# Optimization experiments

Hardware: AMD Instinct MI355X
Metric: run time of the kernel (lower is better)

## Reference

```python
import jax, jax.numpy as jnp
import numpy as np

NUM_HEADS = 16
NUM_KV_HEADS = 4
HEAD_DIM = 128
TOP_K = 4
RMS_EPS = 1e-6
ROPE_THETA = 10000.0


def setup_inputs() -> dict:
    key = jax.random.key(0)
    ks = jax.random.split(key, 10)
    T, h, E, I, SI = 1024, 2048, 16, 512, 1024
    s = 0.02  # weight init scale for numerical sanity
    return {
        "hidden_states": jax.random.normal(ks[0], (T, h), jnp.float32),
        "residual": jax.random.normal(ks[1], (T, h), jnp.float32),
        "rms1_w": jnp.ones((h,), jnp.float32),
        "rms2_w": jnp.ones((h,), jnp.float32),
        "w_qkv": jax.random.normal(ks[2], (h, NUM_HEADS * HEAD_DIM + 2 * NUM_KV_HEADS * HEAD_DIM), jnp.float32) * s,
        "w_dense": jax.random.normal(ks[3], (NUM_HEADS * HEAD_DIM, h), jnp.float32) * s,
        "gate_w": jax.random.normal(ks[4], (h, E), jnp.float32) * s,
        "w13": jax.random.normal(ks[5], (E, h, 2 * I), jnp.float32) * s,
        "w2": jax.random.normal(ks[6], (E, I, h), jnp.float32) * s,
        "sw13": jax.random.normal(ks[7], (h, 2 * SI), jnp.float32) * s,
        "sw2": jax.random.normal(ks[8], (SI, h), jnp.float32) * s,
        "position_ids": jnp.arange(T, dtype=jnp.int32),
    }


def _rmsnorm(x, w, eps=RMS_EPS):
    var = jnp.mean(jnp.square(x), axis=-1, keepdims=True)
    return x * jax.lax.rsqrt(var + eps) * w


def _rope_neox(pos, x):
    # x: [T, H, D]; rotate-half (neox) style over full head_dim
    d = x.shape[-1]
    inv_freq = 1.0 / (ROPE_THETA ** (jnp.arange(0, d, 2, dtype=jnp.float32) / d))  # [d/2]
    ang = pos.astype(jnp.float32)[:, None] * inv_freq  # [T, d/2]
    cos = jnp.cos(ang)[:, None, :]  # [T, 1, d/2]
    sin = jnp.sin(ang)[:, None, :]
    x1, x2 = x[..., : d // 2], x[..., d // 2 :]
    return jnp.concatenate([x1 * cos - x2 * sin, x2 * cos + x1 * sin], axis=-1)


def reference(hidden_states, residual, rms1_w, rms2_w, w_qkv, w_dense,
              gate_w, w13, w2, sw13, sw2, position_ids):
    T, h = hidden_states.shape
    q_size = NUM_HEADS * HEAD_DIM
    kv_size = NUM_KV_HEADS * HEAD_DIM

    # --- input RMSNorm with fused residual add ---
    resid = hidden_states + residual
    x = _rmsnorm(resid, rms1_w)

    # --- attention ---
    qkv = x @ w_qkv
    q = qkv[:, :q_size].reshape(T, NUM_HEADS, HEAD_DIM)
    k = qkv[:, q_size : q_size + kv_size].reshape(T, NUM_KV_HEADS, HEAD_DIM)
    v = qkv[:, q_size + kv_size :].reshape(T, NUM_KV_HEADS, HEAD_DIM)
    q = _rope_neox(position_ids, q)
    k = _rope_neox(position_ids, k)
    rep = NUM_HEADS // NUM_KV_HEADS
    kr = jnp.repeat(k, rep, axis=1)  # [T, H, D]
    vr = jnp.repeat(v, rep, axis=1)
    scale = HEAD_DIM ** -0.5
    scores = jnp.einsum('thd,shd->hts', q, kr) * scale  # [H, T, T]
    causal = jnp.tril(jnp.ones((T, T), dtype=bool))
    scores = jnp.where(causal[None], scores, -1e9)
    probs = jax.nn.softmax(scores, axis=-1)
    ctx = jnp.einsum('hts,shd->thd', probs, vr).reshape(T, q_size)
    attn_out = ctx @ w_dense

    # --- post-attention RMSNorm with fused residual add ---
    resid2 = attn_out + resid
    x2 = _rmsnorm(resid2, rms2_w)

    # --- shared experts (SiLU-and-mul MLP) ---
    gu = x2 @ sw13
    sg, su = jnp.split(gu, 2, axis=-1)
    shared = (jax.nn.silu(sg) * su) @ sw2

    # --- MoE routing: softmax -> top-k -> renormalize ---
    E = gate_w.shape[1]
    router_probs = jax.nn.softmax(x2 @ gate_w, axis=-1)  # [T, E]
    topk_w, topk_ids = jax.lax.top_k(router_probs, TOP_K)
    topk_w = topk_w / jnp.sum(topk_w, axis=-1, keepdims=True)
    comb = jnp.zeros((T, E), x2.dtype).at[jnp.arange(T)[:, None], topk_ids].add(topk_w)

    # --- experts (dense grouped-GEMM equivalent, combined by routing weights) ---
    h_all = jnp.einsum('td,edf->etf', x2, w13)  # [E, T, 2I]
    eg, eu = jnp.split(h_all, 2, axis=-1)
    act = jax.nn.silu(eg) * eu  # [E, T, I]
    moe = jnp.einsum('etf,efh,te->th', act, w2, comb)

    return (moe + shared, resid2)
```

## Files before the change

### kernel.cpp

```cpp
#include <hip/hip_runtime.h>
#include <math.h>

#define HD 2048
#define NQH 16
#define NKVH 4
#define HEADD 128
#define QKVN 3072
#define NEXP 16
#define EI 512
#define SSI 1024
#define TOPK 4
#define TT 1024

typedef __bf16 bf16x8 __attribute__((ext_vector_type(8)));
typedef float f32x4 __attribute__((ext_vector_type(4)));
typedef unsigned short u16x8 __attribute__((ext_vector_type(8)));

static __device__ __forceinline__ unsigned short f2bf(float f) {
    union { float f; unsigned int u; } v; v.f = f;
    unsigned int r = v.u + 0x7fff + ((v.u >> 16) & 1);
    return (unsigned short)(r >> 16);
}

static __device__ __forceinline__ void gl_lds16(const unsigned short* g,
                                                unsigned short* l) {
    __builtin_amdgcn_global_load_lds(
        (const __attribute__((address_space(1))) unsigned int*)g,
        (__attribute__((address_space(3))) unsigned int*)l, 16, 0, 0);
}

__global__ __launch_bounds__(256) void add_rmsnorm_kernel(
    const float* __restrict__ a, const float* __restrict__ b,
    const float* __restrict__ w, float* __restrict__ resid_out,
    unsigned short* __restrict__ x_bf)
{
    int t = blockIdx.x;
    int tid = threadIdx.x;
    const float4* a4 = (const float4*)(a + (size_t)t * HD);
    const float4* b4 = b ? (const float4*)(b + (size_t)t * HD) : nullptr;
    float4* r4 = resid_out ? (float4*)(resid_out + (size_t)t * HD) : nullptr;
    const float4* w4 = (const float4*)w;

    float4 v[2];
    float ss = 0.f;
#pragma unroll
    for (int l = 0; l < 2; ++l) {
        int idx = tid + l * 256;
        float4 va = a4[idx];
        if (b4) {
            float4 vb = b4[idx];
            va.x += vb.x; va.y += vb.y; va.z += vb.z; va.w += vb.w;
        }
        if (r4) r4[idx] = va;
        v[l] = va;
        ss += va.x * va.x + va.y * va.y + va.z * va.z + va.w * va.w;
    }
    for (int off = 32; off > 0; off >>= 1) ss += __shfl_down(ss, off);
    __shared__ float red[4];
    int lane = tid & 63, wv = tid >> 6;
    if (lane == 0) red[wv] = ss;
    __syncthreads();
    if (tid == 0) {
        float s = red[0] + red[1] + red[2] + red[3];
        red[0] = rsqrtf(s / (float)HD + 1e-6f);
    }
    __syncthreads();
    float inv = red[0];
#pragma unroll
    for (int l = 0; l < 2; ++l) {
        int idx = tid + l * 256;
        float4 va = v[l], vw = w4[idx];
        ushort4 ob;
        ob.x = f2bf(va.x * inv * vw.x);
        ob.y = f2bf(va.y * inv * vw.y);
        ob.z = f2bf(va.z * inv * vw.z);
        ob.w = f2bf(va.w * inv * vw.w);
        ((ushort4*)(x_bf + (size_t)t * HD))[idx] = ob;
    }
}

__global__ __launch_bounds__(256) void transpose_convert(
    const float* __restrict__ in, unsigned short* __restrict__ out,
    int K, int N, long long strideIn, long long strideOut)
{
    __shared__ float tile[64][33];
    const int n0 = blockIdx.x * 32;
    const int k0 = blockIdx.y * 64;
    const float* ip = in + (size_t)blockIdx.z * strideIn;
    unsigned short* op = out + (size_t)blockIdx.z * strideOut;
    int tid = threadIdx.x;
    int c = (tid & 7) * 4;
#pragma unroll
    for (int i = 0; i < 2; ++i) {
        int r = (tid >> 3) + i * 32;
        float4 v = *(const float4*)(ip + (size_t)(k0 + r) * N + n0 + c);
        tile[r][c] = v.x; tile[r][c + 1] = v.y;
        tile[r][c + 2] = v.z; tile[r][c + 3] = v.w;
    }
    __syncthreads();
    int rr = tid >> 3;
    int kc = (tid & 7) * 8;
    u16x8 o;
#pragma unroll
    for (int j = 0; j < 8; ++j) o[j] = f2bf(tile[kc + j][rr]);
    *(u16x8*)(op + (size_t)(n0 + rr) * K + k0 + kc) = o;
}

#define SBK 64

__global__ __launch_bounds__(256) void gemm_splitk(
    const unsigned short* __restrict__ A, const unsigned short* __restrict__ B,
    float* __restrict__ Cpart, int M, int N, int Kc, int ldA, int ldB)
{
    __shared__ unsigned short As[2][128 * SBK];
    __shared__ unsigned short Bs[2][128 * SBK];

    const int tid = threadIdx.x;
    const int wave = tid >> 6;
    const int lane = tid & 63;
    const int wr = wave >> 1, wc = wave & 1;
    const int l15 = lane & 15;
    const int row0 = blockIdx.y * 128;
    const int col0 = blockIdx.x * 128;
    const int z = blockIdx.z;

    const unsigned short* Ap = A + (size_t)row0 * ldA + (size_t)z * Kc;
    const unsigned short* Bp = B + (size_t)col0 * ldB + (size_t)z * Kc;

    const int r_st = tid >> 3;
    const int q_st = tid & 7;
    const int csrc = (q_st ^ (r_st & 7)) << 3;

    f32x4 acc[4][4] = {};

    const int nsteps = Kc / SBK;

#define STAGE_SK(buf, k0s)                                                    \
    {                                                                         \
        _Pragma("unroll")                                                     \
        for (int i = 0; i < 4; ++i) {                                         \
            int rr = r_st + i * 32;                                           \
            gl_lds16(Ap + (size_t)rr * ldA + (k0s) + csrc,                    \
                     &As[buf][rr * SBK + q_st * 8]);                          \
            gl_lds16(Bp + (size_t)rr * ldB + (k0s) + csrc,                    \
                     &Bs[buf][rr * SBK + q_st * 8]);                          \
        }                                                                     \
    }

    STAGE_SK(0, 0);

    for (int s = 0; s < nsteps; ++s) {
        const int cur = s & 1;
        if (s + 1 < nsteps) {
            STAGE_SK(cur ^ 1, (s + 1) * SBK);
            asm volatile("s_waitcnt vmcnt(8)" ::: "memory");
        } else {
            asm volatile("s_waitcnt vmcnt(0)" ::: "memory");
        }
        __builtin_amdgcn_s_barrier();

#pragma unroll
        for (int half = 0; half < 2; ++half) {
            const int q = half * 4 + (lane >> 4);
            bf16x8 af[4], bfv[4];
#pragma unroll
            for (int i = 0; i < 4; ++i) {
                int R = wr * 64 + i * 16 + l15;
                af[i] = *(const bf16x8*)&As[cur][R * SBK + ((q ^ (R & 7)) << 3)];
            }
#pragma unroll
            for (int j = 0; j < 4; ++j) {
                int R = wc * 64 + j * 16 + l15;
                bfv[j] = *(const bf16x8*)&Bs[cur][R * SBK + ((q ^ (R & 7)) << 3)];
            }
#pragma unroll
            for (int mi = 0; mi < 4; ++mi)
#pragma unroll
                for (int nj = 0; nj < 4; ++nj)
                    acc[mi][nj] = __builtin_amdgcn_mfma_f32_16x16x32_bf16(
                        af[mi], bfv[nj], acc[mi][nj], 0, 0, 0);
        }
        __builtin_amdgcn_s_barrier();
    }

    float* Cp = Cpart + (size_t)z * M * N;
#pragma unroll
    for (int mi = 0; mi < 4; ++mi)
#pragma unroll
        for (int nj = 0; nj < 4; ++nj)
#pragma unroll
            for (int r = 0; r < 4; ++r) {
                int row = row0 + wr * 64 + mi * 16 + (lane >> 4) * 4 + r;
                int col = col0 + wc * 64 + nj * 16 + l15;
                Cp[(size_t)row * N + col] = acc[mi][nj][r];
            }
}

__global__ __launch_bounds__(256) void reduce_partials(
    const float* __restrict__ part, int ns, int n4,
    const float* __restrict__ add, float* __restrict__ out, int acc)
{
    const float4* p4 = (const float4*)part;
    const float4* a4 = (const float4*)add;
    float4* o4 = (float4*)out;
    for (int idx = blockIdx.x * 256 + threadIdx.x; idx < n4;
         idx += gridDim.x * 256) {
        float4 s = p4[idx];
        for (int z = 1; z < ns; ++z) {
            float4 q = p4[(size_t)z * n4 + idx];
            s.x += q.x; s.y += q.y; s.z += q.z; s.w += q.w;
        }
        if (add) {
            float4 q = a4[idx];
            s.x += q.x; s.y += q.y; s.z += q.z; s.w += q.w;
        }
        if (acc) {
            float4 q = o4[idx];
            s.x += q.x; s.y += q.y; s.z += q.z; s.w += q.w;
        }
        o4[idx] = s;
    }
}

__global__ __launch_bounds__(256) void reduce_swiglu(
    const float* __restrict__ part, int ns, unsigned short* __restrict__ out)
{
    int idx4 = blockIdx.x * 256 + threadIdx.x;
    int t = idx4 >> 8;
    int i4 = (idx4 & 255) * 4;
    const float4* pg = (const float4*)(part + (size_t)t * (2 * SSI) + i4);
    const float4* pu = (const float4*)(part + (size_t)t * (2 * SSI) + SSI + i4);
    float4 g = pg[0], u = pu[0];
    for (int z = 1; z < ns; ++z) {
        float4 g2 = *(const float4*)((const float*)pg + (size_t)z * TT * 2 * SSI);
        float4 u2 = *(const float4*)((const float*)pu + (size_t)z * TT * 2 * SSI);
        g.x += g2.x; g.y += g2.y; g.z += g2.z; g.w += g2.w;
        u.x += u2.x; u.y += u2.y; u.z += u2.z; u.w += u2.w;
    }
    ushort4 o;
    o.x = f2bf((g.x / (1.f + __expf(-g.x))) * u.x);
    o.y = f2bf((g.y / (1.f + __expf(-g.y))) * u.y);
    o.z = f2bf((g.z / (1.f + __expf(-g.z))) * u.z);
    o.w = f2bf((g.w / (1.f + __expf(-g.w))) * u.w);
    *(ushort4*)(out + (size_t)t * SSI + i4) = o;
}

__global__ __launch_bounds__(256) void build_lists(
    const float* __restrict__ comb, int* __restrict__ lists,
    int* __restrict__ slots, int* __restrict__ cnts)
{
    int e = blockIdx.x;
    int tid = threadIdx.x;
    __shared__ int sc[256];
    int loc[4];
    int c = 0;
#pragma unroll
    for (int j = 0; j < 4; ++j) {
        int t = tid * 4 + j;
        if (comb[(size_t)t * NEXP + e] > 0.f) loc[c++] = t;
    }
    sc[tid] = c;
    __syncthreads();
    for (int off = 1; off < 256; off <<= 1) {
        int v = (tid >= off) ? sc[tid - off] : 0;
        __syncthreads();
        sc[tid] += v;
        __syncthreads();
    }
    int base = sc[tid] - c;
    for (int i = 0; i < c; ++i) {
        int t = loc[i];
        int s = 0;
        for (int e2 = 0; e2 < e; ++e2)
            s += (comb[(size_t)t * NEXP + e2] > 0.f) ? 1 : 0;
        lists[e * TT + base + i] = t;
        slots[e * TT + base + i] = s;
    }
    if (tid == 255) cnts[e] = sc[255];
}

__global__ void scan_cnts(const int* __restrict__ cnts, int* __restrict__ bases)
{
    if (threadIdx.x == 0 && blockIdx.x == 0) {
        int a = 0;
        for (int e = 0; e < NEXP; ++e) { bases[e] = a; a += cnts[e]; }
        bases[NEXP] = a;
    }
}

__global__ __launch_bounds__(256) void moe_up_gather(
    const unsigned short* __restrict__ x2B,
    const unsigned short* __restrict__ w13T,
    const float* __restrict__ comb,
    const int* __restrict__ lists,
    const int* __restrict__ cnts,
    const int* __restrict__ bases,
    unsigned short* __restrict__ actC)
{
    __shared__ unsigned short As[3][64 * 64];
    __shared__ unsigned short Bgs[3][64 * 64];
    __shared__ unsigned short Bus[3][64 * 64];

    const int e = blockIdx.z;
    const int cnt = cnts[e];
    const int m0 = blockIdx.y * 64;
    if (m0 >= cnt) return;
    const int n0 = blockIdx.x * 64;
    const int base_e = bases[e];

    const int tid = threadIdx.x;
    const int w = tid >> 6;
    const int lane = tid & 63;
    const int l15 = lane & 15;
    const int g = lane >> 4;

    const int r0 = tid >> 3;
    const int q_st = tid & 7;
    const int swz = (q_st ^ (r0 & 7)) << 3;

    int a0 = m0 + r0, a1 = m0 + r0 + 32;
    int tok0 = lists[e * TT + (a0 < cnt ? a0 : cnt - 1)];
    int tok1 = lists[e * TT + (a1 < cnt ? a1 : cnt - 1)];
    const unsigned short* Asrc0 = x2B + (size_t)tok0 * HD;
    const unsigned short* Asrc1 = x2B + (size_t)tok1 * HD;
    const unsigned short* Bbase = w13T + (size_t)e * 1024 * HD;
    const unsigned short* Bg0 = Bbase + (size_t)(n0 + r0) * HD;
    const unsigned short* Bg1 = Bbase + (size_t)(n0 + r0 + 32) * HD;
    const unsigned short* Bu0 = Bg0 + (size_t)512 * HD;
    const unsigned short* Bu1 = Bg1 + (size_t)512 * HD;

    f32x4 ag[4] = {};
    f32x4 au[4] = {};

#define STAGE_UP(buf, k0s)                                                    \
    {                                                                         \
        gl_lds16(Asrc0 + (k0s) + swz, &As[buf][(tid) * 8]);                   \
        gl_lds16(Asrc1 + (k0s) + swz, &As[buf][(tid + 256) * 8]);             \
        gl_lds16(Bg0 + (k0s) + swz, &Bgs[buf][(tid) * 8]);                    \
        gl_lds16(Bg1 + (k0s) + swz, &Bgs[buf][(tid + 256) * 8]);              \
        gl_lds16(Bu0 + (k0s) + swz, &Bus[buf][(tid) * 8]);                    \
        gl_lds16(Bu1 + (k0s) + swz, &Bus[buf][(tid + 256) * 8]);              \
    }

    const int nsteps = HD / 64;
    STAGE_UP(0, 0);
    STAGE_UP(1, 64);

    for (int s = 0; s < nsteps; ++s) {
        const int cur = s % 3;
        if (s + 2 < nsteps) {
            STAGE_UP((s + 2) % 3, (s + 2) * 64);
            asm volatile("s_waitcnt vmcnt(12)" ::: "memory");
        } else if (s + 1 < nsteps) {
            asm volatile("s_waitcnt vmcnt(6)" ::: "memory");
        } else {
            asm volatile("s_waitcnt vmcnt(0)" ::: "memory");
        }
        __builtin_amdgcn_s_barrier();

#pragma unroll
        for (int kk2 = 0; kk2 < 2; ++kk2) {
            const int q = kk2 * 4 + g;
            bf16x8 af[4], bg, bu;
#pragma unroll
            for (int i = 0; i < 4; ++i) {
                int R = i * 16 + l15;
                af[i] = *(const bf16x8*)&As[cur][R * 64 + ((q ^ (R & 7)) << 3)];
            }
            {
                int R = w * 16 + l15;
                int off = R * 64 + ((q ^ (R & 7)) << 3);
                bg = *(const bf16x8*)&Bgs[cur][off];
                bu = *(const bf16x8*)&Bus[cur][off];
            }
#pragma unroll
            for (int mi = 0; mi < 4; ++mi) {
                ag[mi] = __builtin_amdgcn_mfma_f32_16x16x32_bf16(
                    af[mi], bg, ag[mi], 0, 0, 0);
                au[mi] = __builtin_amdgcn_mfma_f32_16x16x32_bf16(
                    af[mi], bu, au[mi], 0, 0, 0);
            }
        }
        __builtin_amdgcn_s_barrier();
    }

#pragma unroll
    for (int mi = 0; mi < 4; ++mi) {
#pragma unroll
        for (int r = 0; r < 4; ++r) {
            int grow = m0 + mi * 16 + g * 4 + r;
            if (grow >= cnt) continue;
            int tok = lists[e * TT + grow];
            float cw = comb[(size_t)tok * NEXP + e];
            int col = n0 + w * 16 + l15;
            float gg = ag[mi][r];
            float uu = au[mi][r];
            float v = (gg / (1.f + __expf(-gg))) * uu * cw;
            actC[(size_t)(base_e + grow) * EI + col] = f2bf(v);
        }
    }
}

__global__ __launch_bounds__(256) void moe_down_gather(
    const unsigned short* __restrict__ actC,
    const unsigned short* __restrict__ w2T,
    const int* __restrict__ lists,
    const int* __restrict__ slots,
    const int* __restrict__ cnts,
    const int* __restrict__ bases,
    float* __restrict__ slotpart)
{
    __shared__ unsigned short As[3][64 * 64];
    __shared__ unsigned short Bs[3][128 * 64];

    const int e = blockIdx.z;
    const int cnt = cnts[e];
    const int m0 = blockIdx.y * 64;
    if (m0 >= cnt) return;
    const int n0 = blockIdx.x * 128;
    const int base_e = bases[e];

    const int tid = threadIdx.x;
    const int w = tid >> 6;
    const int lane = tid & 63;
    const int l15 = lane & 15;
    const int g = lane >> 4;

    const int r0 = tid >> 3;
    const int q_st = tid & 7;
    const int swz = (q_st ^ (r0 & 7)) << 3;

    int a0 = m0 + r0, a1 = m0 + r0 + 32;
    const unsigned short* Asrc0 =
        actC + (size_t)(base_e + (a0 < cnt ? a0 : cnt - 1)) * EI;
    const unsigned short* Asrc1 =
        actC + (size_t)(base_e + (a1 < cnt ? a1 : cnt - 1)) * EI;
    const unsigned short* Bbase = w2T + (size_t)e * EI;

#define STAGE_DN(buf, k0s)                                                    \
    {                                                                         \
        gl_lds16(Asrc0 + (k0s) + swz, &As[buf][(tid) * 8]);                   \
        gl_lds16(Asrc1 + (k0s) + swz, &As[buf][(tid + 256) * 8]);             \
        _Pragma("unroll")                                                     \
        for (int i = 0; i < 4; ++i) {                                         \
            int rr = r0 + i * 32;                                             \
            gl_lds16(Bbase + (size_t)(n0 + rr) * (NEXP * EI) + (k0s) + swz,   \
                     &Bs[buf][(tid + i * 256) * 8]);                          \
        }                                                                     \
    }

    f32x4 acc[4][2] = {};

    const int nsteps = EI / 64;
    STAGE_DN(0, 0);
    STAGE_DN(1, 64);

    for (int s = 0; s < nsteps; ++s) {
        const int cur = s % 3;
        if (s + 2 < nsteps) {
            STAGE_DN((s + 2) % 3, (s + 2) * 64);
            asm volatile("s_waitcnt vmcnt(12)" ::: "memory");
        } else if (s + 1 < nsteps) {
            asm volatile("s_waitcnt vmcnt(6)" ::: "memory");
        } else {
            asm volatile("s_waitcnt vmcnt(0)" ::: "memory");
        }
        __builtin_amdgcn_s_barrier();

#pragma unroll
        for (int kk2 = 0; kk2 < 2; ++kk2) {
            const int q = kk2 * 4 + g;
            bf16x8 af[4], bf[2];
#pragma unroll
            for (int i = 0; i < 4; ++i) {
                int R = i * 16 + l15;
                af[i] = *(const bf16x8*)&As[cur][R * 64 + ((q ^ (R & 7)) << 3)];
            }
#pragma unroll
            for (int j = 0; j < 2; ++j) {
                int R = w * 32 + j * 16 + l15;
                bf[j] = *(const bf16x8*)&Bs[cur][R * 64 + ((q ^ (R & 7)) << 3)];
            }
#pragma unroll
            for (int mi = 0; mi < 4; ++mi)
#pragma unroll
                for (int nj = 0; nj < 2; ++nj)
                    acc[mi][nj] = __builtin_amdgcn_mfma_f32_16x16x32_bf16(
                        af[mi], bf[nj], acc[mi][nj], 0, 0, 0);
        }
        __builtin_amdgcn_s_barrier();
    }

#pragma unroll
    for (int mi = 0; mi < 4; ++mi) {
#pragma unroll
        for (int r = 0; r < 4; ++r) {
            int grow = m0 + mi * 16 + g * 4 + r;
            if (grow >= cnt) continue;
            int tok = lists[e * TT + grow];
            int sl  = slots[e * TT + grow];
            float* orow = slotpart + (size_t)sl * TT * HD + (size_t)tok * HD;
#pragma unroll
            for (int nj = 0; nj < 2; ++nj) {
                int col = n0 + w * 32 + nj * 16 + l15;
                orow[col] = acc[mi][nj][r];
            }
        }
    }
}

__global__ __launch_bounds__(256) void rope_pack(
    const float* __restrict__ qkv0, const float* __restrict__ qkv1,
    const int* __restrict__ pos_ids,
    unsigned short* __restrict__ Qb, unsigned short* __restrict__ Kb,
    unsigned short* __restrict__ Vb)
{
    const float SCALE = 0.08838834764831843f;
    int t = blockIdx.x;
    int tid = threadIdx.x;
    int w = tid >> 6, lane = tid & 63;
    float pos = (float)pos_ids[t];
    float invf = powf(10000.0f, -(float)lane * (1.0f / 64.0f));
    float ang = pos * invf;
    float c = cosf(ang);
    float s = sinf(ang);
    const float* row0 = qkv0 + (size_t)t * QKVN;
    const float* row1 = qkv1 + (size_t)t * QKVN;
#pragma unroll
    for (int j = 0; j < 5; ++j) {
        int hh = w * 5 + j;
        const float* hb0 = row0 + hh * HEADD;
        const float* hb1 = row1 + hh * HEADD;
        float x1 = hb0[lane] + hb1[lane];
        float x2 = hb0[lane + 64] + hb1[lane + 64];
        float o1 = x1 * c - x2 * s;
        float o2 = x2 * c + x1 * s;
        if (hh < NQH) {
            unsigned short* qp = Qb + ((size_t)hh * TT + t) * HEADD;
            qp[lane] = f2bf(o1 * SCALE);
            qp[lane + 64] = f2bf(o2 * SCALE);
        } else {
            unsigned short* kp = Kb + ((size_t)(hh - NQH) * TT + t) * HEADD;
            kp[lane] = f2bf(o1);
            kp[lane + 64] = f2bf(o2);
        }
    }
    float2 v0 = *(const float2*)(row0 + 2560 + tid * 2);
    float2 v1 = *(const float2*)(row1 + 2560 + tid * 2);
    int kvh = tid >> 6;
    int d = (tid * 2) & 127;
    unsigned int packed = (unsigned int)f2bf(v0.x + v1.x) |
                          ((unsigned int)f2bf(v0.y + v1.y) << 16);
    *(unsigned int*)(Vb + ((size_t)kvh * TT + t) * HEADD + d) = packed;
}

__global__ __launch_bounds__(256) void transpose_v(
    const unsigned short* __restrict__ Vb, unsigned short* __restrict__ Vt)
{
    __shared__ unsigned short tile[32][40];
    const int kvh = blockIdx.z;
    const int t0 = blockIdx.x * 32, d0 = blockIdx.y * 32;
    int tid = threadIdx.x;
    int r = tid >> 3, c4 = (tid & 7) * 4;
    ushort4 v = *(const ushort4*)(Vb + ((size_t)kvh * TT + t0 + r) * HEADD + d0 + c4);
    tile[r][c4] = v.x; tile[r][c4 + 1] = v.y;
    tile[r][c4 + 2] = v.z; tile[r][c4 + 3] = v.w;
    __syncthreads();
    ushort4 o;
    o.x = tile[c4 + 0][r];
    o.y = tile[c4 + 1][r];
    o.z = tile[c4 + 2][r];
    o.w = tile[c4 + 3][r];
    *(ushort4*)(Vt + ((size_t)kvh * HEADD + d0 + r) * TT + t0 + c4) = o;
}

__global__ __launch_bounds__(128) void flash_attn_mfma(
    const unsigned short* __restrict__ Qb,
    const unsigned short* __restrict__ Kb,
    const unsigned short* __restrict__ Vt,
    unsigned short* __restrict__ ctx)
{
    __shared__ __align__(16) unsigned short Ks[2][64 * 128];
    __shared__ __align__(16) unsigned short Vs[2][128 * 64];
    __shared__ __align__(16) unsigned short Pl[2][16][72];

    const int h   = blockIdx.x;
    const int p   = blockIdx.y;
    const int rh  = blockIdx.z;
    const int kvh = h >> 2;
    const int tid = threadIdx.x;
    const int w   = tid >> 6;
    const int lane = tid & 63;
    const int l15 = lane & 15;
    const int g   = lane >> 4;

    const unsigned short* Kh = Kb + (size_t)kvh * TT * HEADD;
    const unsigned short* Vh = Vt + (size_t)kvh * HEADD * TT;

#define STAGE_KV(buf, s0s)                                                    \
    {                                                                         \
        _Pragma("unroll")                                                     \
        for (int i = 0; i < 8; ++i) {                                         \
            int idx = tid + i * 128;                                          \
            int r = idx >> 4, c = idx & 15;                                   \
            int csw = (c & 8) | ((c ^ r) & 7);                                \
            gl_lds16(Kh + (size_t)((s0s) + r) * HEADD + csw * 8,              \
                     &Ks[buf][idx * 8]);                                      \
        }                                                                     \
        _Pragma("unroll")                                                     \
        for (int i = 0; i < 8; ++i) {                                         \
            int idx = tid + i * 128;                                          \
            int r = idx >> 3, c = idx & 7;                                    \
            int csw = (c ^ r) & 7;                                            \
            gl_lds16(Vh + (size_t)r * TT + (s0s) + csw * 8,                   \
                     &Vs[buf][idx * 8]);                                      \
        }                                                                     \
    }

    const int qts[2] = {p, 15 - p};

#pragma unroll
    for (int qi = 0; qi < 2; ++qi) {
        const int qt = qts[qi];
        const int q0 = qt * 64 + rh * 32 + w * 16;
        const int ntiles = qt + 1;

        const unsigned short* Qrow = Qb + ((size_t)h * TT + q0 + l15) * HEADD;
        bf16x8 qf[4];
#pragma unroll
        for (int kk = 0; kk < 4; ++kk)
            qf[kk] = *(const bf16x8*)(Qrow + kk * 32 + g * 8);

        float m_i[4], l_i[4];
#pragma unroll
        for (int r = 0; r < 4; ++r) { m_i[r] = -1e30f; l_i[r] = 0.f; }
        f32x4 of[8] = {};

        STAGE_KV(0, 0);

        for (int st = 0; st < ntiles; ++st) {
            const int cur = st & 1;
            const int s0 = st * 64;
            if (st + 1 < ntiles) {
                STAGE_KV(cur ^ 1, (st + 1) * 64);
                asm volatile("s_waitcnt vmcnt(16)" ::: "memory");
            } else {
                asm volatile("s_waitcnt vmcnt(0)" ::: "memory");
            }
            __builtin_amdgcn_s_barrier();

            f32x4 sacc[4] = {};
#pragma unroll
            for (int kk = 0; kk < 4; ++kk) {
#pragma unroll
                for (int n = 0; n < 4; ++n) {
                    int R = n * 16 + l15;
                    int cidx = kk * 4 + g;
                    int cs = (cidx & 8) | ((cidx ^ R) & 7);
                    bf16x8 kb = *(const bf16x8*)&Ks[cur][R * 128 + cs * 8];
                    sacc[n] = __builtin_amdgcn_mfma_f32_16x16x32_bf16(
                        qf[kk], kb, sacc[n], 0, 0, 0);
                }
            }

            const bool diag = (st == qt);
            float alpha[4];
#pragma unroll
            for (int r = 0; r < 4; ++r) {
                const int qrow = q0 + g * 4 + r;
                float sv[4] = {sacc[0][r], sacc[1][r], sacc[2][r], sacc[3][r]};
                if (diag) {
#pragma unroll
                    for (int n = 0; n < 4; ++n)
                        if (s0 + n * 16 + l15 > qrow) sv[n] = -1e30f;
                }
                float rm = fmaxf(fmaxf(sv[0], sv[1]), fmaxf(sv[2], sv[3]));
                rm = fmaxf(rm, __shfl_xor(rm, 1));
                rm = fmaxf(rm, __shfl_xor(rm, 2));
                rm = fmaxf(rm, __shfl_xor(rm, 4));
                rm = fmaxf(rm, __shfl_xor(rm, 8));
                float mnew = fmaxf(m_i[r], rm);
                alpha[r] = __expf(m_i[r] - mnew);
                float p0 = __expf(sv[0] - mnew);
                float p1 = __expf(sv[1] - mnew);
                float p2 = __expf(sv[2] - mnew);
                float p3 = __expf(sv[3] - mnew);
                float rs = p0 + p1 + p2 + p3;
                rs += __shfl_xor(rs, 1);
                rs += __shfl_xor(rs, 2);
                rs += __shfl_xor(rs, 4);
                rs += __shfl_xor(rs, 8);
                l_i[r] = l_i[r] * alpha[r] + rs;
                m_i[r] = mnew;
                Pl[w][g * 4 + r][0 * 16 + l15] = f2bf(p0);
                Pl[w][g * 4 + r][1 * 16 + l15] = f2bf(p1);
                Pl[w][g * 4 + r][2 * 16 + l15] = f2bf(p2);
                Pl[w][g * 4 + r][3 * 16 + l15] = f2bf(p3);
            }

#pragma unroll
            for (int nd = 0; nd < 8; ++nd)
#pragma unroll
                for (int r = 0; r < 4; ++r)
                    of[nd][r] *= alpha[r];

#pragma unroll
            for (int kk2 = 0; kk2 < 2; ++kk2) {
                bf16x8 pa = *(const bf16x8*)&Pl[w][l15][kk2 * 32 + g * 8];
#pragma unroll
                for (int nd = 0; nd < 8; ++nd) {
                    int R = nd * 16 + l15;
                    int cidx = kk2 * 4 + g;
                    int cs = (cidx ^ R) & 7;
                    bf16x8 vb = *(const bf16x8*)&Vs[cur][R * 64 + cs * 8];
                    of[nd] = __builtin_amdgcn_mfma_f32_16x16x32_bf16(
                        pa, vb, of[nd], 0, 0, 0);
                }
            }
            __builtin_amdgcn_s_barrier();
        }

        float invl[4];
#pragma unroll
        for (int r = 0; r < 4; ++r) invl[r] = 1.f / l_i[r];
#pragma unroll
        for (int nd = 0; nd < 8; ++nd)
#pragma unroll
            for (int r = 0; r < 4; ++r) {
                int trow = q0 + g * 4 + r;
                ctx[(size_t)trow * (NQH * HEADD) + h * HEADD + nd * 16 + l15] =
                    f2bf(of[nd][r] * invl[r]);
            }
    }
}

__global__ __launch_bounds__(256) void router_fused(
    const float* __restrict__ resid2, const float* __restrict__ w,
    const float* __restrict__ gate_w, float* __restrict__ comb)
{
    int t = blockIdx.x;
    int tid = threadIdx.x;
    int lane = tid & 63, wv = tid >> 6;

    const float4* r4 = (const float4*)(resid2 + (size_t)t * HD);
    float4 xa = r4[tid * 2], xb = r4[tid * 2 + 1];
    float ss = xa.x * xa.x + xa.y * xa.y + xa.z * xa.z + xa.w * xa.w +
               xb.x * xb.x + xb.y * xb.y + xb.z * xb.z + xb.w * xb.w;
    for (int off = 32; off > 0; off >>= 1) ss += __shfl_down(ss, off);
    __shared__ float red[4];
    if (lane == 0) red[wv] = ss;
    __syncthreads();
    float inv = rsqrtf((red[0] + red[1] + red[2] + red[3]) / (float)HD + 1e-6f);

    const float4* w4 = (const float4*)w;
    float4 wa = w4[tid * 2], wb = w4[tid * 2 + 1];
    float xs[8] = {xa.x * wa.x * inv, xa.y * wa.y * inv, xa.z * wa.z * inv,
                   xa.w * wa.w * inv, xb.x * wb.x * inv, xb.y * wb.y * inv,
                   xb.z * wb.z * inv, xb.w * wb.w * inv};

    float acc[16] = {};
    int kbase = tid * 8;
#pragma unroll
    for (int j = 0; j < 8; ++j) {
        float xv = xs[j];
        const float4* wrow = (const float4*)(gate_w + (size_t)(kbase + j) * NEXP);
        float4 w0 = wrow[0], w1 = wrow[1], w2 = wrow[2], w3 = wrow[3];
        acc[0] += xv * w0.x;  acc[1] += xv * w0.y;  acc[2] += xv * w0.z;  acc[3] += xv * w0.w;
        acc[4] += xv * w1.x;  acc[5] += xv * w1.y;  acc[6] += xv * w1.z;  acc[7] += xv * w1.w;
        acc[8] += xv * w2.x;  acc[9] += xv * w2.y;  acc[10] += xv * w2.z; acc[11] += xv * w2.w;
        acc[12] += xv * w3.x; acc[13] += xv * w3.y; acc[14] += xv * w3.z; acc[15] += xv * w3.w;
    }
    __shared__ float red2[4][16];
#pragma unroll
    for (int e = 0; e < 16; ++e) {
        float v = acc[e];
        v += __shfl_xor(v, 1);
        v += __shfl_xor(v, 2);
        v += __shfl_xor(v, 4);
        v += __shfl_xor(v, 8);
        v += __shfl_xor(v, 16);
        v += __shfl_xor(v, 32);
        if (lane == 0) red2[wv][e] = v;
    }
    __syncthreads();

    if (tid == 0) {
        float l[NEXP];
#pragma unroll
        for (int e = 0; e < NEXP; ++e)
            l[e] = red2[0][e] + red2[1][e] + red2[2][e] + red2[3][e];
        int sel[TOPK];
        float selv[TOPK];
        bool used[NEXP] = {};
#pragma unroll
        for (int r = 0; r < TOPK; ++r) {
            int best = -1;
            float bv = -1e30f;
            for (int e = 0; e < NEXP; ++e)
                if (!used[e] && l[e] > bv) { bv = l[e]; best = e; }
            used[best] = true;
            sel[r] = best;
            selv[r] = bv;
        }
        float mx = selv[0];
        float wsum = 0.f, wvv[TOPK];
#pragma unroll
        for (int r = 0; r < TOPK; ++r) { wvv[r] = __expf(selv[r] - mx); wsum += wvv[r]; }
        float out16[NEXP] = {};
#pragma unroll
        for (int r = 0; r < TOPK; ++r) out16[sel[r]] = wvv[r] / wsum;
#pragma unroll
        for (int e = 0; e < NEXP; ++e) comb[(size_t)t * NEXP + e] = out16[e];
    }
}

extern "C" void kernel_launch(void* const* d_in, const int* in_sizes, int n_in,
                              void* d_out, int out_size, void* d_ws, size_t ws_size,
                              hipStream_t stream)
{
    const float* hidden   = (const float*)d_in[0];
    const float* residual = (const float*)d_in[1];
    const float* rms1_w   = (const float*)d_in[2];
    const float* rms2_w   = (const float*)d_in[3];
    const float* w_qkv    = (const float*)d_in[4];
    const float* w_dense  = (const float*)d_in[5];
    const float* gate_w   = (const float*)d_in[6];
    const float* w13      = (const float*)d_in[7];
    const float* w2       = (const float*)d_in[8];
    const float* sw13     = (const float*)d_in[9];
    const float* sw2      = (const float*)d_in[10];
    const int*   pos_ids  = (const int*)d_in[11];

    const int T = TT;

    float* out0 = (float*)d_out;
    float* out1 = (float*)d_out + (size_t)T * HD;

    char* base = (char*)d_ws;
    float*          residF = (float*)(base);
    unsigned short* xB     = (unsigned short*)(base + 8388608);
    unsigned short* ctxB   = (unsigned short*)(base + 12582912);
    unsigned short* actC   = (unsigned short*)(base);
    unsigned short* x2B    = (unsigned short*)(base + 29360128);
    unsigned short* sactB  = (unsigned short*)(base + 33554432);
    float*          comb   = (float*)(base + 35651584);
    float*          part   = (float*)(base + 35717120);
    unsigned short* Wbuf   = (unsigned short*)(base + 69271552);
    int*            lists  = (int*)(base + 139526144);
    int*            cnts   = (int*)(base + 139591680);
    int*            slots  = (int*)(base + 139591936);
    int*            bases  = (int*)(base + 139657472);

    unsigned short* Qb = (unsigned short*)(base + 35717120 + 25165824);
    unsigned short* Kb = Qb + (size_t)NQH * TT * HEADD;
    unsigned short* Vb = Kb + (size_t)NKVH * TT * HEADD;
    unsigned short* Vt = Vb + (size_t)NKVH * TT * HEADD;

    dim3 blk(256);

    add_rmsnorm_kernel<<<dim3(T), blk, 0, stream>>>(
        hidden, residual, rms1_w, residF, xB);

    transpose_convert<<<dim3(QKVN / 32, HD / 64), blk, 0, stream>>>(
        w_qkv, Wbuf, HD, QKVN, 0, 0);
    gemm_splitk<<<dim3(QKVN / 128, T / 128, 2), blk, 0, stream>>>(
        xB, Wbuf, part, T, QKVN, 1024, HD, HD);

    rope_pack<<<dim3(T), blk, 0, stream>>>(
        part, part + (size_t)T * QKVN, pos_ids, Qb, Kb, Vb);
    transpose_v<<<dim3(T / 32, HEADD / 32, NKVH), blk, 0, stream>>>(Vb, Vt);

    flash_attn_mfma<<<dim3(NQH, 8, 2), dim3(128), 0, stream>>>(Qb, Kb, Vt, ctxB);

    transpose_convert<<<dim3(HD / 32, HD / 64), blk, 0, stream>>>(
        w_dense, Wbuf, HD, HD, 0, 0);
    gemm_splitk<<<dim3(HD / 128, T / 128, 4), blk, 0, stream>>>(
        ctxB, Wbuf, part, T, HD, 512, HD, HD);
    reduce_partials<<<dim3(1024), blk, 0, stream>>>(
        part, 4, T * HD / 4, residF, out1, 0);

    add_rmsnorm_kernel<<<dim3(T), blk, 0, stream>>>(
        out1, nullptr, rms2_w, nullptr, x2B);

    router_fused<<<dim3(T), blk, 0, stream>>>(out1, rms2_w, gate_w, comb);
    build_lists<<<dim3(NEXP), blk, 0, stream>>>(comb, lists, slots, cnts);
    scan_cnts<<<dim3(1), dim3(64), 0, stream>>>(cnts, bases);

    transpose_convert<<<dim3(2 * SSI / 32, HD / 64), blk, 0, stream>>>(
        sw13, Wbuf, HD, 2 * SSI, 0, 0);
    gemm_splitk<<<dim3(HD / 128, T / 128, 4), blk, 0, stream>>>(
        x2B, Wbuf, part, T, 2 * SSI, 512, HD, HD);

    reduce_swiglu<<<dim3(T * SSI / 4 / 256), blk, 0, stream>>>(part, 4, sactB);

    transpose_convert<<<dim3(HD / 32, SSI / 64), blk, 0, stream>>>(
        sw2, Wbuf, SSI, HD, 0, 0);
    gemm_splitk<<<dim3(HD / 128, T / 128, 4), blk, 0, stream>>>(
        sactB, Wbuf, part, T, HD, 256, SSI, SSI);
    reduce_partials<<<dim3(1024), blk, 0, stream>>>(
        part, 4, T * HD / 4, nullptr, out0, 0);

    transpose_convert<<<dim3(1024 / 32, HD / 64, NEXP), blk, 0, stream>>>(
        w13, Wbuf, HD, 1024, (long long)HD * 1024, (long long)1024 * HD);
    moe_up_gather<<<dim3(EI / 64, 16, NEXP), blk, 0, stream>>>(
        x2B, Wbuf, comb, lists, cnts, bases, actC);

    transpose_convert<<<dim3(HD / 32, (NEXP * EI) / 64), blk, 0, stream>>>(
        w2, Wbuf, NEXP * EI, HD, 0, 0);
    moe_down_gather<<<dim3(HD / 128, 16, NEXP), blk, 0, stream>>>(
        actC, Wbuf, lists, slots, cnts, bases, part);
    reduce_partials<<<dim3(1024), blk, 0, stream>>>(
        part, 4, T * HD / 4, nullptr, out0, 1);
}
```

Measured before the change: 367.9 us.

## Fuse split-K reduce with residual add and RMSNorm; double-buffer MoE GEMMs

Replaces the reduce_partials plus add_rmsnorm pair after the dense projection with one kernel. It sums the four split-K partials, adds the residual, writes resid2 and emits the bf16 normalized activations, which saves a launch and a round trip of the fp32 activations through memory. The MoE up and down gather GEMMs also drop from triple to double LDS buffering. That lowers shared memory per block and may allow more resident blocks, but it gives less prefetch depth to hide global-load latency.

```diff
diff --git a/kernel.cpp b/kernel.cpp
--- a/kernel.cpp
+++ b/kernel.cpp
@@ -76,6 +76,60 @@
         ob.z = f2bf(va.z * inv * vw.z);
         ob.w = f2bf(va.w * inv * vw.w);
         ((ushort4*)(x_bf + (size_t)t * HD))[idx] = ob;
+    }
+}
+
+__global__ __launch_bounds__(256) void reduce4_add_rmsnorm(
+    const float* __restrict__ part, const float* __restrict__ resid,
+    const float* __restrict__ w, float* __restrict__ resid2_out,
+    unsigned short* __restrict__ x_bf)
+{
+    const size_t NP = (size_t)TT * HD / 4;
+    int t = blockIdx.x;
+    int tid = threadIdx.x;
+    const float4* p4 = (const float4*)part;
+    const float4* r4 = (const float4*)(resid + (size_t)t * HD);
+    float4* o4 = (float4*)(resid2_out + (size_t)t * HD);
+    const float4* w4 = (const float4*)w;
+
+    float4 v[2];
+    float ss = 0.f;
+#pragma unroll
+    for (int l = 0; l < 2; ++l) {
+        int li = tid + l * 256;
+        size_t idx = (size_t)t * (HD / 4) + li;
+        float4 s = p4[idx];
+        float4 q1 = p4[NP + idx], q2 = p4[2 * NP + idx], q3 = p4[3 * NP + idx];
+        float4 rr = r4[li];
+        s.x += q1.x + q2.x + q3.x + rr.x;
+        s.y += q1.y + q2.y + q3.y + rr.y;
+        s.z += q1.z + q2.z + q3.z + rr.z;
+        s.w += q1.w + q2.w + q3.w + rr.w;
+        o4[li] = s;
+        v[l] = s;
+        ss += s.x * s.x + s.y * s.y + s.z * s.z + s.w * s.w;
+    }
+    for (int off = 32; off > 0; off >>= 1) ss += __shfl_down(ss, off);
+    __shared__ float red[4];
+    int lane = tid & 63, wv = tid >> 6;
+    if (lane == 0) red[wv] = ss;
+    __syncthreads();
+    if (tid == 0) {
+        float s = red[0] + red[1] + red[2] + red[3];
+        red[0] = rsqrtf(s / (float)HD + 1e-6f);
+    }
+    __syncthreads();
+    float inv = red[0];
+#pragma unroll
+    for (int l = 0; l < 2; ++l) {
+        int li = tid + l * 256;
+        float4 va = v[l], vw = w4[li];
+        ushort4 ob;
+        ob.x = f2bf(va.x * inv * vw.x);
+        ob.y = f2bf(va.y * inv * vw.y);
+        ob.z = f2bf(va.z * inv * vw.z);
+        ob.w = f2bf(va.w * inv * vw.w);
+        ((ushort4*)(x_bf + (size_t)t * HD))[li] = ob;
     }
 }
 
@@ -297,9 +351,9 @@
     const int* __restrict__ bases,
     unsigned short* __restrict__ actC)
 {
-    __shared__ unsigned short As[3][64 * 64];
-    __shared__ unsigned short Bgs[3][64 * 64];
-    __shared__ unsigned short Bus[3][64 * 64];
+    __shared__ unsigned short As[2][64 * 64];
+    __shared__ unsigned short Bgs[2][64 * 64];
+    __shared__ unsigned short Bus[2][64 * 64];
 
     const int e = blockIdx.z;
     const int cnt = cnts[e];
@@ -342,16 +396,13 @@
         gl_lds16(Bu1 + (k0s) + swz, &Bus[buf][(tid + 256) * 8]);              \
     }
 
+    STAGE_UP(0, 0);
+
     const int nsteps = HD / 64;
-    STAGE_UP(0, 0);
-    STAGE_UP(1, 64);
-
     for (int s = 0; s < nsteps; ++s) {
-        const int cur = s % 3;
-        if (s + 2 < nsteps) {
-            STAGE_UP((s + 2) % 3, (s + 2) * 64);
-            asm volatile("s_waitcnt vmcnt(12)" ::: "memory");
-        } else if (s + 1 < nsteps) {
+        const int cur = s & 1;
+        if (s + 1 < nsteps) {
+            STAGE_UP(cur ^ 1, (s + 1) * 64);
             asm volatile("s_waitcnt vmcnt(6)" ::: "memory");
         } else {
             asm volatile("s_waitcnt vmcnt(0)" ::: "memory");
@@ -410,8 +461,8 @@
     const int* __restrict__ bases,
     float* __restrict__ slotpart)
 {
-    __shared__ unsigned short As[3][64 * 64];
-    __shared__ unsigned short Bs[3][128 * 64];
+    __shared__ unsigned short As[2][64 * 64];
+    __shared__ unsigned short Bs[2][128 * 64];
 
     const int e = blockIdx.z;
     const int cnt = cnts[e];
@@ -451,16 +502,13 @@
 
     f32x4 acc[4][2] = {};
 
+    STAGE_DN(0, 0);
+
     const int nsteps = EI / 64;
-    STAGE_DN(0, 0);
-    STAGE_DN(1, 64);
-
     for (int s = 0; s < nsteps; ++s) {
-        const int cur = s % 3;
-        if (s + 2 < nsteps) {
-            STAGE_DN((s + 2) % 3, (s + 2) * 64);
-            asm volatile("s_waitcnt vmcnt(12)" ::: "memory");
-        } else if (s + 1 < nsteps) {
+        const int cur = s & 1;
+        if (s + 1 < nsteps) {
+            STAGE_DN(cur ^ 1, (s + 1) * 64);
             asm volatile("s_waitcnt vmcnt(6)" ::: "memory");
         } else {
             asm volatile("s_waitcnt vmcnt(0)" ::: "memory");
@@ -876,11 +924,8 @@
         w_dense, Wbuf, HD, HD, 0, 0);
     gemm_splitk<<<dim3(HD / 128, T / 128, 4), blk, 0, stream>>>(
         ctxB, Wbuf, part, T, HD, 512, HD, HD);
-    reduce_partials<<<dim3(1024), blk, 0, stream>>>(
-        part, 4, T * HD / 4, residF, out1, 0);
-
-    add_rmsnorm_kernel<<<dim3(T), blk, 0, stream>>>(
-        out1, nullptr, rms2_w, nullptr, x2B);
+    reduce4_add_rmsnorm<<<dim3(T), blk, 0, stream>>>(
+        part, residF, rms2_w, out1, x2B);
 
     router_fused<<<dim3(T), blk, 0, stream>>>(out1, rms2_w, gate_w, comb);
     build_lists<<<dim3(NEXP), blk, 0, stream>>>(comb, lists, slots, cnts);
```

After: 350.1 us (median of 3 runs). -4.8%, faster.
